# Performance work log

Measured on AMD Instinct MI355X. Metric: run time of the kernel, lower is better.

The kernel has to match this reference:

```python
import jax, jax.numpy as jnp
import numpy as np

Nn, Nt, Np, Ne = 100000, 30000, 400000, 1000000
IN_NODE, IN_NET, IN_PIN, IN_EDGE = 16, 8, 8, 4
H, HP, HE, L, T = 64, 16, 8, 3, 4
LOG2 = 0.6931471805599453  # ShiftedSoftplus shift


def _lrelu(x):
    return jax.nn.leaky_relu(x, 0.01)


def _ssp(x):  # DGL ShiftedSoftplus: softplus(x) - log(2)
    return jax.nn.softplus(x) - LOG2


def _forward(in_node_feat, in_net_feat, in_pin_feat, in_edge_feat,
             pins_src, pins_dst, near_src, near_dst,
             node_lin_W, node_lin_b, net_lin_W, net_lin_b,
             pin_lin_W, pin_lin_b, edge_lin_W, edge_lin_b,
             geom_W, geom_b, pins_W, pins_b,
             cf_node_W, cf_node_b, cf_e1_W, cf_e1_b, cf_e2_W, cf_e2_b,
             cf_out_W, cf_out_b, sage_pool_W, sage_pool_b,
             sage_self_W, sage_neigh_W, sage_bias,
             out1_W, out1_b, out2_W, out2_b, out3_W, out3_b,
             outn1_W, outn1_b, outn2_W, outn2_b, outn3_W, outn3_b):
    node_feat = _lrelu(in_node_feat @ node_lin_W + node_lin_b)   # [Nn,H]
    net_feat = _lrelu(in_net_feat @ net_lin_W + net_lin_b)       # [Nt,H]
    pin_feat = _lrelu(in_pin_feat @ pin_lin_W + pin_lin_b)       # [Np,HP]
    edge_feat = _lrelu(in_edge_feat @ edge_lin_W + edge_lin_b)   # [Ne,HE]

    # static degree norms for GraphConv(norm='both') on 'pins' (node->net)
    ones_p = jnp.ones((Np,), jnp.float32)
    deg_out = jax.ops.segment_sum(ones_p, pins_src, num_segments=Nn)
    deg_in = jax.ops.segment_sum(ones_p, pins_dst, num_segments=Nt)
    src_norm = jnp.clip(deg_out, 1.0, None) ** -0.5
    dst_norm = jnp.clip(deg_in, 1.0, None) ** -0.5

    for i in range(L):
        # --- 'pins' GraphConv (node -> net), norm='both' ---
        msg = (node_feat * src_norm[:, None])[pins_src]                 # [Np,H]
        agg = jax.ops.segment_sum(msg, pins_dst, num_segments=Nt)      # [Nt,H]
        net_out = (agg * dst_norm[:, None]) @ pins_W[i] + pins_b[i]

        # --- 'pinned' CFConv (net -> node), reverse pins, edge feats = pin_feat ---
        hv = net_feat @ cf_node_W[i] + cf_node_b[i]                    # [Nt,H]
        he = _ssp(pin_feat @ cf_e1_W[i] + cf_e1_b[i])
        he = _ssp(he @ cf_e2_W[i] + cf_e2_b[i])                        # [Np,H]
        m = hv[pins_dst] * he                                          # src of 'pinned' = pins_dst
        h_cf = jax.ops.segment_sum(m, pins_src, num_segments=Nn)       # dst of 'pinned' = pins_src
        node_cf = _ssp(h_cf @ cf_out_W[i] + cf_out_b[i])

        # --- 'near' SAGEConv(pool) with sigmoid edge weights ---
        ew = jax.nn.sigmoid(edge_feat @ geom_W[i] + geom_b[i])         # [Ne,1]
        hp = jax.nn.relu(node_feat @ sage_pool_W[i] + sage_pool_b[i])  # [Nn,H]
        m2 = hp[near_src] * ew                                         # [Ne,H], nonnegative
        h_neigh = jax.ops.segment_max(m2, near_dst, num_segments=Nn)
        h_neigh = jnp.maximum(h_neigh, 0.0)  # zero-degree nodes -> 0 (msgs are >= 0)
        node_sage = node_feat @ sage_self_W[i] + h_neigh @ sage_neigh_W[i] + sage_bias[i]

        # hetero max-aggregation over edge types hitting dst 'node'
        node_feat = _lrelu(jnp.maximum(node_cf, node_sage))
        net_feat = _lrelu(net_out)

    h = _lrelu(jnp.concatenate([in_node_feat, node_feat], axis=-1) @ out1_W + out1_b)
    h = _lrelu(h @ out2_W + out2_b)
    node_pred = jax.nn.sigmoid(h @ out3_W + out3_b)
    g = _lrelu(jnp.concatenate([in_net_feat, net_feat], axis=-1) @ outn1_W + outn1_b)
    g = _lrelu(g @ outn2_W + outn2_b)
    net_pred = jax.nn.sigmoid(g @ outn3_W + outn3_b)
    return node_pred, net_pred


def setup_inputs() -> dict:
    key = jax.random.key(0)
    ks = iter(jax.random.split(key, 80))

    def nrm(shape, scale=0.05):
        return jax.random.normal(next(ks), shape, jnp.float32) * scale

    inp = {}
    inp['in_node_feat'] = nrm((Nn, IN_NODE), 1.0)
    inp['in_net_feat'] = nrm((Nt, IN_NET), 1.0)
    inp['in_pin_feat'] = nrm((Np, IN_PIN), 1.0)
    inp['in_edge_feat'] = nrm((Ne, IN_EDGE), 1.0)
    inp['pins_src'] = jax.random.randint(next(ks), (Np,), 0, Nn)
    inp['pins_dst'] = jax.random.randint(next(ks), (Np,), 0, Nt)
    inp['near_src'] = jax.random.randint(next(ks), (Ne,), 0, Nn)
    inp['near_dst'] = jax.random.randint(next(ks), (Ne,), 0, Nn)
    inp['node_lin_W'] = nrm((IN_NODE, H)); inp['node_lin_b'] = nrm((H,))
    inp['net_lin_W'] = nrm((IN_NET, H)); inp['net_lin_b'] = nrm((H,))
    inp['pin_lin_W'] = nrm((IN_PIN, HP)); inp['pin_lin_b'] = nrm((HP,))
    inp['edge_lin_W'] = nrm((IN_EDGE, HE)); inp['edge_lin_b'] = nrm((HE,))
    inp['geom_W'] = nrm((L, HE, 1)); inp['geom_b'] = nrm((L, 1))
    inp['pins_W'] = nrm((L, H, H)); inp['pins_b'] = nrm((L, H))
    inp['cf_node_W'] = nrm((L, H, H)); inp['cf_node_b'] = nrm((L, H))
    inp['cf_e1_W'] = nrm((L, HP, H)); inp['cf_e1_b'] = nrm((L, H))
    inp['cf_e2_W'] = nrm((L, H, H)); inp['cf_e2_b'] = nrm((L, H))
    inp['cf_out_W'] = nrm((L, H, H)); inp['cf_out_b'] = nrm((L, H))
    inp['sage_pool_W'] = nrm((L, H, H)); inp['sage_pool_b'] = nrm((L, H))
    inp['sage_self_W'] = nrm((L, H, H))
    inp['sage_neigh_W'] = nrm((L, H, H))
    inp['sage_bias'] = nrm((L, H))
    inp['out1_W'] = nrm((IN_NODE + H, H)); inp['out1_b'] = nrm((H,))
    inp['out2_W'] = nrm((H, H)); inp['out2_b'] = nrm((H,))
    inp['out3_W'] = nrm((H, T)); inp['out3_b'] = nrm((T,))
    inp['outn1_W'] = nrm((IN_NET + H, H)); inp['outn1_b'] = nrm((H,))
    inp['outn2_W'] = nrm((H, H)); inp['outn2_b'] = nrm((H,))
    inp['outn3_W'] = nrm((H, 1)); inp['outn3_b'] = nrm((1,))
    return inp


def reference(in_node_feat, in_net_feat, in_pin_feat, in_edge_feat,
              pins_src, pins_dst, near_src, near_dst,
              node_lin_W, node_lin_b, net_lin_W, net_lin_b,
              pin_lin_W, pin_lin_b, edge_lin_W, edge_lin_b,
              geom_W, geom_b, pins_W, pins_b,
              cf_node_W, cf_node_b, cf_e1_W, cf_e1_b, cf_e2_W, cf_e2_b,
              cf_out_W, cf_out_b, sage_pool_W, sage_pool_b,
              sage_self_W, sage_neigh_W, sage_bias,
              out1_W, out1_b, out2_W, out2_b, out3_W, out3_b,
              outn1_W, outn1_b, outn2_W, outn2_b, outn3_W, outn3_b):
    return _forward(in_node_feat, in_net_feat, in_pin_feat, in_edge_feat,
                    pins_src, pins_dst, near_src, near_dst,
                    node_lin_W, node_lin_b, net_lin_W, net_lin_b,
                    pin_lin_W, pin_lin_b, edge_lin_W, edge_lin_b,
                    geom_W, geom_b, pins_W, pins_b,
                    cf_node_W, cf_node_b, cf_e1_W, cf_e1_b, cf_e2_W, cf_e2_b,
                    cf_out_W, cf_out_b, sage_pool_W, sage_pool_b,
                    sage_self_W, sage_neigh_W, sage_bias,
                    out1_W, out1_b, out2_W, out2_b, out3_W, out3_b,
                    outn1_W, outn1_b, outn2_W, outn2_b, outn3_W, outn3_b)
```

## Files before the change

### kernel.cpp

```cpp
#include <hip/hip_runtime.h>
#include <hip/hip_bf16.h>

#define DEV __device__ __forceinline__

DEV float lrelu_(float x){ return x > 0.f ? x : 0.01f * x; }
DEV float ssp_(float x){ return fmaxf(x, 0.f) + __logf(1.f + __expf(-fabsf(x))) - 0.69314718055994530942f; }
DEV float sigm_(float x){ return 1.f / (1.f + __expf(-x)); }

DEV unsigned short f2bf(float x){
    unsigned int u = __float_as_uint(x);
    unsigned int r = (u + 0x7FFFu + ((u >> 16) & 1u)) >> 16;
    return (unsigned short)r;
}
DEV float bf2f(unsigned short s){ return __uint_as_float((unsigned int)s << 16); }
DEV ushort4 pack4(float4 v){
    ushort4 u; u.x = f2bf(v.x); u.y = f2bf(v.y); u.z = f2bf(v.z); u.w = f2bf(v.w); return u;
}

DEV void fma44(float (&acc)[4][4], const float4 (&xa)[4], const float4 (&wa)[4])
{
    #pragma unroll
    for (int kk = 0; kk < 4; kk++) {
        #pragma unroll
        for (int i = 0; i < 4; i++) {
            float x = ((const float*)&xa[i])[kk];
            #pragma unroll
            for (int j = 0; j < 4; j++)
                acc[i][j] += x * ((const float*)&wa[kk])[j];
        }
    }
}

typedef short s8v __attribute__((ext_vector_type(8)));
typedef float f4v __attribute__((ext_vector_type(4)));

template<int K, int ACT, bool OUTBF>
__global__ __launch_bounds__(256) void gemm64_kernel(const float* __restrict__ X,
                                                     const float* __restrict__ W,
                                                     const float* __restrict__ B,
                                                     void* __restrict__ Yv, int nrows)
{
    constexpr int XS = K + 4;
    constexpr int KQ = K / 4;
    __shared__ float Ws[K * 64];
    __shared__ float bs[64];
    __shared__ float Xs[64 * XS];
    for (int i = threadIdx.x; i < K * 64; i += 256) Ws[i] = W[i];
    if (threadIdx.x < 64) bs[threadIdx.x] = B[threadIdx.x];
    const int tr = threadIdx.x >> 4, tc = threadIdx.x & 15;
    const int r0 = tr * 4, c0 = tc * 4;
    for (int base = blockIdx.x * 64; base < nrows; base += gridDim.x * 64) {
        __syncthreads();
        for (int i = threadIdx.x; i < 64 * KQ; i += 256) {
            int row = i / KQ, kq = (i % KQ) * 4;
            int g = base + row;
            float4 v = make_float4(0.f, 0.f, 0.f, 0.f);
            if (g < nrows) v = *(const float4*)&X[(size_t)g * K + kq];
            *(float4*)&Xs[row * XS + kq] = v;
        }
        __syncthreads();
        float acc[4][4];
        #pragma unroll
        for (int i = 0; i < 4; i++)
            #pragma unroll
            for (int j = 0; j < 4; j++) acc[i][j] = bs[c0 + j];
        #pragma unroll 4
        for (int kq = 0; kq < K; kq += 4) {
            float4 xa[4], wa[4];
            #pragma unroll
            for (int i = 0; i < 4; i++) xa[i] = *(const float4*)&Xs[(r0 + i) * XS + kq];
            #pragma unroll
            for (int j = 0; j < 4; j++) wa[j] = *(const float4*)&Ws[(kq + j) * 64 + c0];
            fma44(acc, xa, wa);
        }
        #pragma unroll
        for (int i = 0; i < 4; i++) {
            int g = base + r0 + i;
            if (g < nrows) {
                float4 o;
                float* op = (float*)&o;
                #pragma unroll
                for (int j = 0; j < 4; j++) {
                    float a = acc[i][j];
                    if (ACT == 1) a = lrelu_(a);
                    else if (ACT == 2) a = fmaxf(a, 0.f);
                    op[j] = a;
                }
                if (OUTBF) *(ushort4*)&((unsigned short*)Yv)[(size_t)g * 64 + c0] = pack4(o);
                else       *(float4*)&((float*)Yv)[(size_t)g * 64 + c0] = o;
            }
        }
    }
}

template<int ACT, bool INBF, bool OUTBF>
__global__ __launch_bounds__(256) void mfma_gemm_kernel(const void* __restrict__ Xv,
                                                        const float* __restrict__ W,
                                                        const float* __restrict__ B,
                                                        void* __restrict__ Yv, int nrows)
{
    __shared__ __align__(16) unsigned short WT[64 * 72];
    __shared__ __align__(16) unsigned short Axs[64 * 72];
    __shared__ float bs[64];
    for (int i = threadIdx.x; i < 4096; i += 256) {
        int k = i >> 6, nn = i & 63;
        WT[nn * 72 + k] = f2bf(W[i]);
    }
    if (threadIdx.x < 64) bs[threadIdx.x] = B[threadIdx.x];
    const int lane = threadIdx.x & 63, wv = threadIdx.x >> 6;
    const int l15 = lane & 15, quad = lane >> 4;
    const int arow = 16 * wv + l15;
    const int koff = quad * 8;
    for (int base = blockIdx.x * 64; base < nrows; base += gridDim.x * 64) {
        __syncthreads();
        {
            int row = threadIdx.x >> 2, kq = (threadIdx.x & 3) * 16;
            int g = base + row;
            if (INBF) {
                const unsigned short* Xb = (const unsigned short*)Xv;
                uint4 v0 = make_uint4(0,0,0,0), v1 = v0;
                if (g < nrows) {
                    v0 = *(const uint4*)&Xb[(size_t)g * 64 + kq];
                    v1 = *(const uint4*)&Xb[(size_t)g * 64 + kq + 8];
                }
                *(uint4*)&Axs[row * 72 + kq] = v0;
                *(uint4*)&Axs[row * 72 + kq + 8] = v1;
            } else {
                const float* Xf = (const float*)Xv;
                #pragma unroll
                for (int m = 0; m < 4; m++) {
                    float4 v = make_float4(0,0,0,0);
                    if (g < nrows) v = *(const float4*)&Xf[(size_t)g * 64 + kq + m * 4];
                    *(ushort4*)&Axs[row * 72 + kq + m * 4] = pack4(v);
                }
            }
        }
        __syncthreads();
        f4v acc[4];
        #pragma unroll
        for (int t = 0; t < 4; t++) acc[t] = (f4v){0.f,0.f,0.f,0.f};
        s8v a0 = *(const s8v*)&Axs[arow * 72 + koff];
        s8v a1 = *(const s8v*)&Axs[arow * 72 + 32 + koff];
        #pragma unroll
        for (int t = 0; t < 4; t++) {
            int nn = t * 16 + l15;
            s8v b0 = *(const s8v*)&WT[nn * 72 + koff];
            s8v b1 = *(const s8v*)&WT[nn * 72 + 32 + koff];
            acc[t] = __builtin_amdgcn_mfma_f32_16x16x32_bf16(a0, b0, acc[t], 0, 0, 0);
            acc[t] = __builtin_amdgcn_mfma_f32_16x16x32_bf16(a1, b1, acc[t], 0, 0, 0);
        }
        const int mrow = 16 * wv + quad * 4;
        #pragma unroll
        for (int t = 0; t < 4; t++) {
            int col = t * 16 + l15;
            float b = bs[col];
            #pragma unroll
            for (int r = 0; r < 4; r++) {
                int g = base + mrow + r;
                if (g < nrows) {
                    float a = acc[t][r] + b;
                    if (ACT == 1) a = lrelu_(a);
                    else if (ACT == 2) a = fmaxf(a, 0.f);
                    if (OUTBF) ((unsigned short*)Yv)[(size_t)g * 64 + col] = f2bf(a);
                    else       ((float*)Yv)[(size_t)g * 64 + col] = a;
                }
            }
        }
    }
}

__global__ __launch_bounds__(256) void mfma_combine_kernel(const float* __restrict__ h_cf,
                                                           const unsigned short* __restrict__ nfb,
                                                           const unsigned short* __restrict__ ngb,
                                                           const float* __restrict__ Wc, const float* __restrict__ cB,
                                                           const float* __restrict__ sW, const float* __restrict__ nW,
                                                           const float* __restrict__ sB,
                                                           unsigned short* __restrict__ outb, int n)
{
    __shared__ __align__(16) unsigned short WcT[64 * 72], WsT[64 * 72], WnT[64 * 72];
    __shared__ __align__(16) unsigned short Ac[32 * 72], As[32 * 72], An[32 * 72];
    __shared__ float bc[64], bsg[64];
    for (int i = threadIdx.x; i < 4096; i += 256) {
        int k = i >> 6, nn = i & 63;
        WcT[nn * 72 + k] = f2bf(Wc[i]);
        WsT[nn * 72 + k] = f2bf(sW[i]);
        WnT[nn * 72 + k] = f2bf(nW[i]);
    }
    if (threadIdx.x < 64) { bc[threadIdx.x] = cB[threadIdx.x]; bsg[threadIdx.x] = sB[threadIdx.x]; }
    const int lane = threadIdx.x & 63, wv = threadIdx.x >> 6;
    const int l15 = lane & 15, quad = lane >> 4;
    const int arow = (wv & 1) * 16 + l15;
    const int ct0 = (wv >> 1) * 2;
    const int koff = quad * 8;
    for (int base = blockIdx.x * 32; base < n; base += gridDim.x * 32) {
        __syncthreads();
        {
            int row = threadIdx.x >> 3, kq = (threadIdx.x & 7) * 8;
            int g = base + row;
            float4 c0v = make_float4(0,0,0,0), c1 = c0v;
            uint4 vf = make_uint4(0,0,0,0), vg = vf;
            if (g < n) {
                const float* pc = &h_cf[(size_t)g * 64 + kq];
                c0v = *(const float4*)pc; c1 = *(const float4*)(pc + 4);
                vf = *(const uint4*)&nfb[(size_t)g * 64 + kq];
                vg = *(const uint4*)&ngb[(size_t)g * 64 + kq];
            }
            *(ushort4*)&Ac[row * 72 + kq] = pack4(c0v);
            *(ushort4*)&Ac[row * 72 + kq + 4] = pack4(c1);
            *(uint4*)&As[row * 72 + kq] = vf;
            *(uint4*)&An[row * 72 + kq] = vg;
        }
        __syncthreads();
        f4v accC[2], accS[2];
        #pragma unroll
        for (int t = 0; t < 2; t++) { accC[t] = (f4v){0.f,0.f,0.f,0.f}; accS[t] = (f4v){0.f,0.f,0.f,0.f}; }
        s8v ac0 = *(const s8v*)&Ac[arow * 72 + koff];
        s8v ac1 = *(const s8v*)&Ac[arow * 72 + 32 + koff];
        s8v as0 = *(const s8v*)&As[arow * 72 + koff];
        s8v as1 = *(const s8v*)&As[arow * 72 + 32 + koff];
        s8v an0 = *(const s8v*)&An[arow * 72 + koff];
        s8v an1 = *(const s8v*)&An[arow * 72 + 32 + koff];
        #pragma unroll
        for (int t = 0; t < 2; t++) {
            int nn = (ct0 + t) * 16 + l15;
            s8v wc0 = *(const s8v*)&WcT[nn * 72 + koff];
            s8v wc1 = *(const s8v*)&WcT[nn * 72 + 32 + koff];
            accC[t] = __builtin_amdgcn_mfma_f32_16x16x32_bf16(ac0, wc0, accC[t], 0, 0, 0);
            accC[t] = __builtin_amdgcn_mfma_f32_16x16x32_bf16(ac1, wc1, accC[t], 0, 0, 0);
            s8v ws0 = *(const s8v*)&WsT[nn * 72 + koff];
            s8v ws1 = *(const s8v*)&WsT[nn * 72 + 32 + koff];
            accS[t] = __builtin_amdgcn_mfma_f32_16x16x32_bf16(as0, ws0, accS[t], 0, 0, 0);
            accS[t] = __builtin_amdgcn_mfma_f32_16x16x32_bf16(as1, ws1, accS[t], 0, 0, 0);
            s8v wn0 = *(const s8v*)&WnT[nn * 72 + koff];
            s8v wn1 = *(const s8v*)&WnT[nn * 72 + 32 + koff];
            accS[t] = __builtin_amdgcn_mfma_f32_16x16x32_bf16(an0, wn0, accS[t], 0, 0, 0);
            accS[t] = __builtin_amdgcn_mfma_f32_16x16x32_bf16(an1, wn1, accS[t], 0, 0, 0);
        }
        const int mrow = (wv & 1) * 16 + quad * 4;
        #pragma unroll
        for (int t = 0; t < 2; t++) {
            int col = (ct0 + t) * 16 + l15;
            float bcv = bc[col], bsv = bsg[col];
            #pragma unroll
            for (int r = 0; r < 4; r++) {
                int g = base + mrow + r;
                if (g < n)
                    outb[(size_t)g * 64 + col] = f2bf(lrelu_(fmaxf(ssp_(accC[t][r] + bcv), accS[t][r] + bsv)));
            }
        }
    }
}

template<int K, int C, int ACT>
__global__ __launch_bounds__(256) void lin_kernel(const float* __restrict__ X,
                                                  const float* __restrict__ W,
                                                  const float* __restrict__ B,
                                                  float* __restrict__ Y, int nrows)
{
    constexpr int ROWS = 256 / C;
    __shared__ float Ws[K * C];
    __shared__ float bs[C];
    __shared__ float Xs[ROWS * K];
    for (int i = threadIdx.x; i < K * C; i += 256) Ws[i] = W[i];
    if (threadIdx.x < C) bs[threadIdx.x] = B[threadIdx.x];
    __syncthreads();
    const int r = threadIdx.x / C, c = threadIdx.x % C;
    for (int base = blockIdx.x * ROWS; base < nrows; base += gridDim.x * ROWS) {
        __syncthreads();
        for (int i = threadIdx.x; i < ROWS * K; i += 256) {
            int rr = base + i / K;
            Xs[i] = (rr < nrows) ? X[(size_t)rr * K + i % K] : 0.f;
        }
        __syncthreads();
        int row = base + r;
        if (row < nrows) {
            float acc = bs[c];
            #pragma unroll
            for (int k = 0; k < K; k++) acc += Xs[r * K + k] * Ws[k * C + c];
            if (ACT == 1) acc = lrelu_(acc);
            else if (ACT == 2) acc = fmaxf(acc, 0.f);
            Y[(size_t)row * C + c] = acc;
        }
    }
}

__global__ __launch_bounds__(256) void deg_kernel(const int* __restrict__ src, const int* __restrict__ dst,
                                                  int* __restrict__ degs, int* __restrict__ degd, int np)
{
    int p = blockIdx.x * 256 + threadIdx.x;
    if (p < np) { atomicAdd(&degs[src[p]], 1); atomicAdd(&degd[dst[p]], 1); }
}

__global__ __launch_bounds__(256) void norm_kernel(int* __restrict__ arr, int n)
{
    int i = blockIdx.x * 256 + threadIdx.x;
    if (i < n) {
        int v = arr[i]; if (v < 1) v = 1;
        arr[i] = __float_as_int(rsqrtf((float)v));
    }
}

__global__ __launch_bounds__(256) void csr_count_kernel(const int* __restrict__ key, int* __restrict__ cnt, int ne)
{
    int e = blockIdx.x * 256 + threadIdx.x;
    if (e < ne) atomicAdd(&cnt[key[e]], 1);
}

__global__ __launch_bounds__(256) void scan_block_sum_kernel(const int* __restrict__ cnt, int* __restrict__ bsum, int n)
{
    __shared__ int sh[256];
    int i = blockIdx.x * 256 + threadIdx.x;
    sh[threadIdx.x] = (i < n) ? cnt[i] : 0;
    __syncthreads();
    for (int s = 128; s > 0; s >>= 1) {
        if (threadIdx.x < s) sh[threadIdx.x] += sh[threadIdx.x + s];
        __syncthreads();
    }
    if (threadIdx.x == 0) bsum[blockIdx.x] = sh[0];
}

__global__ __launch_bounds__(512) void scan_bsum_kernel(int* __restrict__ bsum, int nb, int* __restrict__ total_out)
{
    __shared__ int sh[512];
    int i = threadIdx.x;
    int v = (i < nb) ? bsum[i] : 0;
    sh[i] = v;
    __syncthreads();
    for (int s = 1; s < 512; s <<= 1) {
        int add = (i >= s) ? sh[i - s] : 0;
        __syncthreads();
        sh[i] += add;
        __syncthreads();
    }
    if (i < nb) bsum[i] = sh[i] - v;
    if (i == nb - 1) *total_out = sh[i];
}

__global__ __launch_bounds__(256) void scan_final_kernel(const int* __restrict__ cnt, const int* __restrict__ bsum,
                                                         int* __restrict__ row_start, int* __restrict__ nxt, int n)
{
    __shared__ int sh[256];
    int i = blockIdx.x * 256 + threadIdx.x;
    int v = (i < n) ? cnt[i] : 0;
    sh[threadIdx.x] = v;
    __syncthreads();
    for (int s = 1; s < 256; s <<= 1) {
        int add = (threadIdx.x >= s) ? sh[threadIdx.x - s] : 0;
        __syncthreads();
        sh[threadIdx.x] += add;
        __syncthreads();
    }
    if (i < n) {
        int excl = sh[threadIdx.x] - v + bsum[blockIdx.x];
        row_start[i] = excl;
        nxt[i] = excl;
    }
}

__global__ __launch_bounds__(256) void csr_fill_kernel(const int* __restrict__ key, int* __restrict__ nxt,
                                                       int* __restrict__ eidx, int ne)
{
    int e = blockIdx.x * 256 + threadIdx.x;
    if (e < ne) {
        int slot = atomicAdd(&nxt[key[e]], 1);
        eidx[slot] = e;
    }
}

__global__ __launch_bounds__(256) void edge_ew_kernel(const float* __restrict__ in_edge,
                                                      const float* __restrict__ elW, const float* __restrict__ elb,
                                                      const float* __restrict__ gW, const float* __restrict__ gb,
                                                      float* __restrict__ ew3, int ne)
{
    __shared__ float W[32], B[8], G[24], Gb[3];
    if (threadIdx.x < 32) W[threadIdx.x] = elW[threadIdx.x];
    if (threadIdx.x < 8)  B[threadIdx.x] = elb[threadIdx.x];
    if (threadIdx.x < 24) G[threadIdx.x] = gW[threadIdx.x];
    if (threadIdx.x < 3)  Gb[threadIdx.x] = gb[threadIdx.x];
    __syncthreads();
    for (int e = blockIdx.x * 256 + threadIdx.x; e < ne; e += gridDim.x * 256) {
        float4 x = *(const float4*)&in_edge[(size_t)e * 4];
        float ef[8];
        #pragma unroll
        for (int j = 0; j < 8; j++)
            ef[j] = lrelu_(B[j] + x.x * W[j] + x.y * W[8 + j] + x.z * W[16 + j] + x.w * W[24 + j]);
        #pragma unroll
        for (int i = 0; i < 3; i++) {
            float a = Gb[i];
            #pragma unroll
            for (int j = 0; j < 8; j++) a += ef[j] * G[i * 8 + j];
            ew3[(size_t)i * ne + e] = sigm_(a);
        }
    }
}

__global__ __launch_bounds__(256) void pins_gather_kernel(const unsigned short* __restrict__ nfb,
                                                          const float* __restrict__ snorm,
                                                          const float* __restrict__ dnorm,
                                                          const int* __restrict__ psrc,
                                                          const int* __restrict__ prow,
                                                          const int* __restrict__ peidx,
                                                          unsigned short* __restrict__ aggb, int nt)
{
    __shared__ int sS[4][64];
    __shared__ float sN[4][64];
    const int lane = threadIdx.x & 63, wv = threadIdx.x >> 6;
    for (int d = blockIdx.x * 4 + wv; d < nt; d += gridDim.x * 4) {
        int rs = prow[d], re = prow[d + 1];
        float acc = 0.f;
        for (int cbase = rs; cbase < re; cbase += 64) {
            int cnt = re - cbase; if (cnt > 64) cnt = 64;
            if (lane < cnt) {
                int p = peidx[cbase + lane];
                int s = psrc[p];
                sS[wv][lane] = s;
                sN[wv][lane] = snorm[s];
            }
            int k = 0;
            for (; k + 3 < cnt; k += 4) {
                int s0 = sS[wv][k], s1 = sS[wv][k+1], s2 = sS[wv][k+2], s3 = sS[wv][k+3];
                float n0 = sN[wv][k], n1 = sN[wv][k+1], n2 = sN[wv][k+2], n3 = sN[wv][k+3];
                float v0 = bf2f(nfb[(size_t)s0 * 64 + lane]) * n0;
                float v1 = bf2f(nfb[(size_t)s1 * 64 + lane]) * n1;
                float v2 = bf2f(nfb[(size_t)s2 * 64 + lane]) * n2;
                float v3 = bf2f(nfb[(size_t)s3 * 64 + lane]) * n3;
                acc += (v0 + v1) + (v2 + v3);
            }
            for (; k < cnt; k++)
                acc += bf2f(nfb[(size_t)sS[wv][k] * 64 + lane]) * sN[wv][k];
        }
        aggb[(size_t)d * 64 + lane] = f2bf(acc * dnorm[d]);
    }
}

__global__ __launch_bounds__(256) void cf_pin5_kernel(const float* __restrict__ pinf,
                                                      const unsigned short* __restrict__ hvb,
                                                      const int* __restrict__ psrc, const int* __restrict__ pdst,
                                                      const float* __restrict__ W1, const float* __restrict__ B1,
                                                      const float* __restrict__ W2, const float* __restrict__ B2,
                                                      float* __restrict__ h_cf, int np)
{
    __shared__ float Ws1[16 * 64], bs1[64], bs2[64];
    __shared__ __align__(16) unsigned short W2T[64 * 72];
    __shared__ __align__(16) unsigned short T1s[64 * 72];
    __shared__ float PF[64 * 20];
    __shared__ int srcS[64], dstS[64];
    for (int i = threadIdx.x; i < 16 * 64; i += 256) Ws1[i] = W1[i];
    for (int i = threadIdx.x; i < 64 * 64; i += 256) {
        int k = i >> 6, n = i & 63;
        W2T[n * 72 + k] = f2bf(W2[i]);
    }
    if (threadIdx.x < 64) { bs1[threadIdx.x] = B1[threadIdx.x]; bs2[threadIdx.x] = B2[threadIdx.x]; }
    const int tr = threadIdx.x >> 4, tc = threadIdx.x & 15;
    const int r0 = tr * 4, c0 = tc * 4;
    const int lane = threadIdx.x & 63, wv = threadIdx.x >> 6;
    const int l15 = lane & 15, quad = lane >> 4;
    const int arow = 16 * wv + l15;
    const int koff = quad * 8;
    for (int base = blockIdx.x * 64; base < np; base += gridDim.x * 64) {
        __syncthreads();
        {
            int row = threadIdx.x >> 2, kq = (threadIdx.x & 3) * 4;
            int p = base + row;
            float4 v = make_float4(0.f, 0.f, 0.f, 0.f);
            if (p < np) v = *(const float4*)&pinf[(size_t)p * 16 + kq];
            *(float4*)&PF[row * 20 + kq] = v;
            if (threadIdx.x < 64) {
                int pp = base + threadIdx.x;
                srcS[threadIdx.x] = (pp < np) ? psrc[pp] : 0;
                dstS[threadIdx.x] = (pp < np) ? pdst[pp] : 0;
            }
        }
        __syncthreads();
        {
            float acc[4][4];
            #pragma unroll
            for (int i = 0; i < 4; i++)
                #pragma unroll
                for (int j = 0; j < 4; j++) acc[i][j] = bs1[c0 + j];
            #pragma unroll
            for (int kq = 0; kq < 16; kq += 4) {
                float4 xa[4], wa[4];
                #pragma unroll
                for (int i = 0; i < 4; i++) xa[i] = *(const float4*)&PF[(r0 + i) * 20 + kq];
                #pragma unroll
                for (int j = 0; j < 4; j++) wa[j] = *(const float4*)&Ws1[(kq + j) * 64 + c0];
                fma44(acc, xa, wa);
            }
            #pragma unroll
            for (int i = 0; i < 4; i++) {
                ushort4 o;
                o.x = f2bf(ssp_(acc[i][0]));
                o.y = f2bf(ssp_(acc[i][1]));
                o.z = f2bf(ssp_(acc[i][2]));
                o.w = f2bf(ssp_(acc[i][3]));
                *(ushort4*)&T1s[(r0 + i) * 72 + c0] = o;
            }
        }
        __syncthreads();
        {
            f4v acc4[4];
            #pragma unroll
            for (int t = 0; t < 4; t++) acc4[t] = (f4v){0.f, 0.f, 0.f, 0.f};
            s8v a0 = *(const s8v*)&T1s[arow * 72 + koff];
            s8v a1 = *(const s8v*)&T1s[arow * 72 + 32 + koff];
            #pragma unroll
            for (int t = 0; t < 4; t++) {
                int n = t * 16 + l15;
                s8v b0 = *(const s8v*)&W2T[n * 72 + koff];
                s8v b1 = *(const s8v*)&W2T[n * 72 + 32 + koff];
                acc4[t] = __builtin_amdgcn_mfma_f32_16x16x32_bf16(a0, b0, acc4[t], 0, 0, 0);
                acc4[t] = __builtin_amdgcn_mfma_f32_16x16x32_bf16(a1, b1, acc4[t], 0, 0, 0);
            }
            __syncthreads();
            const int mrow = 16 * wv + quad * 4;
            #pragma unroll
            for (int t = 0; t < 4; t++) {
                int col = t * 16 + l15;
                float b = bs2[col];
                #pragma unroll
                for (int r = 0; r < 4; r++)
                    T1s[(mrow + r) * 72 + col] = f2bf(ssp_(acc4[t][r] + b));
            }
        }
        __syncthreads();
        #pragma unroll 4
        for (int i = 0; i < 16; i++) {
            int pl = wv * 16 + i;
            int p = base + pl;
            if (p < np) {
                float m = bf2f(hvb[(size_t)dstS[pl] * 64 + lane]) * bf2f(T1s[pl * 72 + lane]);
                unsafeAtomicAdd(&h_cf[(size_t)srcS[pl] * 64 + lane], m);
            }
        }
    }
}

__global__ __launch_bounds__(256) void sage_gather_kernel(const unsigned short* __restrict__ hpb,
                                                          const float* __restrict__ ew,
                                                          const int* __restrict__ esrc,
                                                          const int* __restrict__ row_start,
                                                          const int* __restrict__ eidx,
                                                          unsigned short* __restrict__ ngb, int nn)
{
    __shared__ int sS[4][64];
    __shared__ float sWt[4][64];
    const int lane = threadIdx.x & 63, wv = threadIdx.x >> 6;
    for (int d = blockIdx.x * 4 + wv; d < nn; d += gridDim.x * 4) {
        int rs = row_start[d], re = row_start[d + 1];
        float acc = 0.f;
        for (int cbase = rs; cbase < re; cbase += 64) {
            int cnt = re - cbase; if (cnt > 64) cnt = 64;
            if (lane < cnt) {
                int e = eidx[cbase + lane];
                sS[wv][lane] = esrc[e];
                sWt[wv][lane] = ew[e];
            }
            int k = 0;
            for (; k + 3 < cnt; k += 4) {
                int s0 = sS[wv][k], s1 = sS[wv][k+1], s2 = sS[wv][k+2], s3 = sS[wv][k+3];
                float w0 = sWt[wv][k], w1 = sWt[wv][k+1], w2 = sWt[wv][k+2], w3 = sWt[wv][k+3];
                float v0 = bf2f(hpb[(size_t)s0 * 64 + lane]) * w0;
                float v1 = bf2f(hpb[(size_t)s1 * 64 + lane]) * w1;
                float v2 = bf2f(hpb[(size_t)s2 * 64 + lane]) * w2;
                float v3 = bf2f(hpb[(size_t)s3 * 64 + lane]) * w3;
                acc = fmaxf(acc, fmaxf(fmaxf(v0, v1), fmaxf(v2, v3)));
            }
            for (; k < cnt; k++)
                acc = fmaxf(acc, bf2f(hpb[(size_t)sS[wv][k] * 64 + lane]) * sWt[wv][k]);
        }
        ngb[(size_t)d * 64 + lane] = f2bf(acc);
    }
}

__global__ __launch_bounds__(256) void node_head3_kernel(const float* __restrict__ in_node,
                                                         const unsigned short* __restrict__ nfb,
                                                         const float* __restrict__ W1, const float* __restrict__ B1,
                                                         const float* __restrict__ W2, const float* __restrict__ B2,
                                                         const float* __restrict__ W3, const float* __restrict__ B3,
                                                         float* __restrict__ out, int n)
{
    __shared__ float Ws1[80 * 64], Ws2[64 * 64], Ws3[64 * 4];
    __shared__ float bs1[64], bs2[64], bs3[4];
    __shared__ float Xs[32 * 84];
    __shared__ float H1[32 * 68];
    for (int i = threadIdx.x; i < 80 * 64; i += 256) Ws1[i] = W1[i];
    for (int i = threadIdx.x; i < 64 * 64; i += 256) Ws2[i] = W2[i];
    for (int i = threadIdx.x; i < 64 * 4; i += 256) Ws3[i] = W3[i];
    if (threadIdx.x < 64) { bs1[threadIdx.x] = B1[threadIdx.x]; bs2[threadIdx.x] = B2[threadIdx.x]; }
    if (threadIdx.x < 4) bs3[threadIdx.x] = B3[threadIdx.x];
    const int tr = threadIdx.x >> 4, tc = threadIdx.x & 15;
    const int r0 = tr * 2, c0 = tc * 4;
    for (int base = blockIdx.x * 32; base < n; base += gridDim.x * 32) {
        __syncthreads();
        for (int i = threadIdx.x; i < 32 * 4; i += 256) {
            int row = i >> 2, kq = (i & 3) * 4;
            int g = base + row;
            float4 v = make_float4(0,0,0,0);
            if (g < n) v = *(const float4*)&in_node[(size_t)g * 16 + kq];
            *(float4*)&Xs[row * 84 + kq] = v;
        }
        for (int i = threadIdx.x; i < 32 * 16; i += 256) {
            int row = i >> 4, kq = (i & 15) * 4;
            int g = base + row;
            float4 v = make_float4(0,0,0,0);
            if (g < n) {
                ushort4 u = *(const ushort4*)&nfb[(size_t)g * 64 + kq];
                v.x = bf2f(u.x); v.y = bf2f(u.y); v.z = bf2f(u.z); v.w = bf2f(u.w);
            }
            *(float4*)&Xs[row * 84 + 16 + kq] = v;
        }
        __syncthreads();
        {
            float acc[2][4];
            #pragma unroll
            for (int i = 0; i < 2; i++)
                #pragma unroll
                for (int j = 0; j < 4; j++) acc[i][j] = bs1[c0 + j];
            #pragma unroll 4
            for (int kq = 0; kq < 80; kq += 4) {
                float4 xa[2], wa[4];
                #pragma unroll
                for (int i = 0; i < 2; i++) xa[i] = *(const float4*)&Xs[(r0 + i) * 84 + kq];
                #pragma unroll
                for (int j = 0; j < 4; j++) wa[j] = *(const float4*)&Ws1[(kq + j) * 64 + c0];
                #pragma unroll
                for (int kk = 0; kk < 4; kk++)
                    #pragma unroll
                    for (int i = 0; i < 2; i++) {
                        float x = ((const float*)&xa[i])[kk];
                        #pragma unroll
                        for (int j = 0; j < 4; j++) acc[i][j] += x * ((const float*)&wa[kk])[j];
                    }
            }
            #pragma unroll
            for (int i = 0; i < 2; i++) {
                float4 o; float* op = (float*)&o;
                #pragma unroll
                for (int j = 0; j < 4; j++) op[j] = lrelu_(acc[i][j]);
                *(float4*)&H1[(r0 + i) * 68 + c0] = o;
            }
        }
        __syncthreads();
        float* H2 = Xs;
        {
            float acc[2][4];
            #pragma unroll
            for (int i = 0; i < 2; i++)
                #pragma unroll
                for (int j = 0; j < 4; j++) acc[i][j] = bs2[c0 + j];
            #pragma unroll 4
            for (int kq = 0; kq < 64; kq += 4) {
                float4 xa[2], wa[4];
                #pragma unroll
                for (int i = 0; i < 2; i++) xa[i] = *(const float4*)&H1[(r0 + i) * 68 + kq];
                #pragma unroll
                for (int j = 0; j < 4; j++) wa[j] = *(const float4*)&Ws2[(kq + j) * 64 + c0];
                #pragma unroll
                for (int kk = 0; kk < 4; kk++)
                    #pragma unroll
                    for (int i = 0; i < 2; i++) {
                        float x = ((const float*)&xa[i])[kk];
                        #pragma unroll
                        for (int j = 0; j < 4; j++) acc[i][j] += x * ((const float*)&wa[kk])[j];
                    }
            }
            __syncthreads();
            #pragma unroll
            for (int i = 0; i < 2; i++) {
                float4 o; float* op = (float*)&o;
                #pragma unroll
                for (int j = 0; j < 4; j++) op[j] = lrelu_(acc[i][j]);
                *(float4*)&H2[(r0 + i) * 68 + c0] = o;
            }
        }
        __syncthreads();
        if (threadIdx.x < 128) {
            int row = threadIdx.x >> 2, c = threadIdx.x & 3;
            float acc = bs3[c];
            #pragma unroll 4
            for (int kq = 0; kq < 64; kq += 4) {
                float4 h = *(const float4*)&H2[row * 68 + kq];
                #pragma unroll
                for (int j = 0; j < 4; j++) acc += ((const float*)&h)[j] * Ws3[(kq + j) * 4 + c];
            }
            int g = base + row;
            if (g < n) out[(size_t)g * 4 + c] = sigm_(acc);
        }
    }
}

__global__ __launch_bounds__(256) void net_head3_kernel(const float* __restrict__ in_net, const float* __restrict__ tf,
                                                        const float* __restrict__ W1, const float* __restrict__ B1,
                                                        const float* __restrict__ W2, const float* __restrict__ B2,
                                                        const float* __restrict__ W3, const float* __restrict__ B3,
                                                        float* __restrict__ out, int n)
{
    __shared__ float Ws1[72 * 64], Ws2[64 * 64], Ws3[64];
    __shared__ float bs1[64], bs2[64], bs3[1];
    __shared__ float Xs[32 * 76];
    __shared__ float H1[32 * 68];
    for (int i = threadIdx.x; i < 72 * 64; i += 256) Ws1[i] = W1[i];
    for (int i = threadIdx.x; i < 64 * 64; i += 256) Ws2[i] = W2[i];
    if (threadIdx.x < 64) { Ws3[threadIdx.x] = W3[threadIdx.x]; bs1[threadIdx.x] = B1[threadIdx.x]; bs2[threadIdx.x] = B2[threadIdx.x]; }
    if (threadIdx.x == 0) bs3[0] = B3[0];
    const int tr = threadIdx.x >> 4, tc = threadIdx.x & 15;
    const int r0 = tr * 2, c0 = tc * 4;
    for (int base = blockIdx.x * 32; base < n; base += gridDim.x * 32) {
        __syncthreads();
        for (int i = threadIdx.x; i < 32 * 2; i += 256) {
            int row = i >> 1, kq = (i & 1) * 4;
            int g = base + row;
            float4 v = make_float4(0,0,0,0);
            if (g < n) v = *(const float4*)&in_net[(size_t)g * 8 + kq];
            *(float4*)&Xs[row * 76 + kq] = v;
        }
        for (int i = threadIdx.x; i < 32 * 16; i += 256) {
            int row = i >> 4, kq = (i & 15) * 4;
            int g = base + row;
            float4 v = make_float4(0,0,0,0);
            if (g < n) v = *(const float4*)&tf[(size_t)g * 64 + kq];
            *(float4*)&Xs[row * 76 + 8 + kq] = v;
        }
        __syncthreads();
        {
            float acc[2][4];
            #pragma unroll
            for (int i = 0; i < 2; i++)
                #pragma unroll
                for (int j = 0; j < 4; j++) acc[i][j] = bs1[c0 + j];
            #pragma unroll 4
            for (int kq = 0; kq < 72; kq += 4) {
                float4 xa[2], wa[4];
                #pragma unroll
                for (int i = 0; i < 2; i++) xa[i] = *(const float4*)&Xs[(r0 + i) * 76 + kq];
                #pragma unroll
                for (int j = 0; j < 4; j++) wa[j] = *(const float4*)&Ws1[(kq + j) * 64 + c0];
                #pragma unroll
                for (int kk = 0; kk < 4; kk++)
                    #pragma unroll
                    for (int i = 0; i < 2; i++) {
                        float x = ((const float*)&xa[i])[kk];
                        #pragma unroll
                        for (int j = 0; j < 4; j++) acc[i][j] += x * ((const float*)&wa[kk])[j];
                    }
            }
            #pragma unroll
            for (int i = 0; i < 2; i++) {
                float4 o; float* op = (float*)&o;
                #pragma unroll
                for (int j = 0; j < 4; j++) op[j] = lrelu_(acc[i][j]);
                *(float4*)&H1[(r0 + i) * 68 + c0] = o;
            }
        }
        __syncthreads();
        float* H2 = Xs;
        {
            float acc[2][4];
            #pragma unroll
            for (int i = 0; i < 2; i++)
                #pragma unroll
                for (int j = 0; j < 4; j++) acc[i][j] = bs2[c0 + j];
            #pragma unroll 4
            for (int kq = 0; kq < 64; kq += 4) {
                float4 xa[2], wa[4];
                #pragma unroll
                for (int i = 0; i < 2; i++) xa[i] = *(const float4*)&H1[(r0 + i) * 68 + kq];
                #pragma unroll
                for (int j = 0; j < 4; j++) wa[j] = *(const float4*)&Ws2[(kq + j) * 64 + c0];
                #pragma unroll
                for (int kk = 0; kk < 4; kk++)
                    #pragma unroll
                    for (int i = 0; i < 2; i++) {
                        float x = ((const float*)&xa[i])[kk];
                        #pragma unroll
                        for (int j = 0; j < 4; j++) acc[i][j] += x * ((const float*)&wa[kk])[j];
                    }
            }
            __syncthreads();
            #pragma unroll
            for (int i = 0; i < 2; i++) {
                float4 o; float* op = (float*)&o;
                #pragma unroll
                for (int j = 0; j < 4; j++) op[j] = lrelu_(acc[i][j]);
                *(float4*)&H2[(r0 + i) * 68 + c0] = o;
            }
        }
        __syncthreads();
        if (threadIdx.x < 32) {
            int row = threadIdx.x;
            float acc = bs3[0];
            #pragma unroll 4
            for (int kq = 0; kq < 64; kq += 4) {
                float4 h = *(const float4*)&H2[row * 68 + kq];
                float4 w = *(const float4*)&Ws3[kq];
                acc += h.x * w.x + h.y * w.y + h.z * w.z + h.w * w.w;
            }
            int g = base + row;
            if (g < n) out[g] = sigm_(acc);
        }
    }
}

extern "C" void kernel_launch(void* const* d_in, const int* in_sizes, int n_in,
                              void* d_out, int out_size, void* d_ws, size_t ws_size,
                              hipStream_t stream)
{
    (void)in_sizes; (void)n_in; (void)out_size; (void)ws_size;
    constexpr int Nn = 100000, Nt = 30000, Np = 400000, Ne = 1000000;
    constexpr int H = 64, L = 3, T = 4;

    auto fpt = [&](int i){ return (const float*)d_in[i]; };
    auto ipt = [&](int i){ return (const int*)d_in[i]; };

    const float* in_node = fpt(0);
    const float* in_net  = fpt(1);
    const float* in_pin  = fpt(2);
    const float* in_edge = fpt(3);
    const int* psrc = ipt(4);
    const int* pdst = ipt(5);
    const int* esrc = ipt(6);
    const int* edst = ipt(7);

    float* ws = (float*)d_ws;
    size_t o = 0;
    auto alloc = [&](size_t nel){ float* p = ws + o; o += nel; return p; };
    unsigned short* node_a = (unsigned short*)alloc((size_t)Nn * 32);
    unsigned short* node_b = (unsigned short*)alloc((size_t)Nn * 32);
    unsigned short* aggb   = (unsigned short*)alloc((size_t)Nt * 32);
    unsigned short* hvb    = (unsigned short*)alloc((size_t)Nt * 32);
    unsigned short* hpb    = (unsigned short*)alloc((size_t)Nn * 32);
    unsigned short* ngb    = (unsigned short*)alloc((size_t)Nn * 32);
    float* net_a  = alloc((size_t)Nt * H);
    float* net_b  = alloc((size_t)Nt * H);
    float* pinf   = alloc((size_t)Np * 16);
    float* h_cf   = alloc((size_t)Nn * H);
    float* ew3    = alloc((size_t)3 * Ne);
    float* snorm  = alloc((size_t)Nn);
    float* dnorm  = alloc((size_t)Nt);
    int* cnt       = (int*)alloc((size_t)Nn);
    int* row_start = (int*)alloc((size_t)Nn + 1);
    int* nxt       = (int*)alloc((size_t)Nn);
    int* eidx      = (int*)alloc((size_t)Ne);
    int* bsum      = (int*)alloc((size_t)512);
    int* pcnt      = (int*)alloc((size_t)Nt);
    int* prow      = (int*)alloc((size_t)Nt + 1);
    int* pnxt      = (int*)alloc((size_t)Nt);
    int* peidx     = (int*)alloc((size_t)Np);
    int* pbsum     = (int*)alloc((size_t)256);

    constexpr int NB  = (Nn + 255) / 256;
    constexpr int NB2 = (Nt + 255) / 256;

    hipMemsetAsync(snorm, 0, (size_t)Nn * 4, stream);
    hipMemsetAsync(dnorm, 0, (size_t)Nt * 4, stream);
    deg_kernel<<<(Np + 255) / 256, 256, 0, stream>>>(psrc, pdst, (int*)snorm, (int*)dnorm, Np);
    norm_kernel<<<(Nn + 255) / 256, 256, 0, stream>>>((int*)snorm, Nn);
    norm_kernel<<<(Nt + 255) / 256, 256, 0, stream>>>((int*)dnorm, Nt);

    hipMemsetAsync(cnt, 0, (size_t)Nn * 4, stream);
    csr_count_kernel<<<(Ne + 255) / 256, 256, 0, stream>>>(edst, cnt, Ne);
    scan_block_sum_kernel<<<NB, 256, 0, stream>>>(cnt, bsum, Nn);
    scan_bsum_kernel<<<1, 512, 0, stream>>>(bsum, NB, row_start + Nn);
    scan_final_kernel<<<NB, 256, 0, stream>>>(cnt, bsum, row_start, nxt, Nn);
    csr_fill_kernel<<<(Ne + 255) / 256, 256, 0, stream>>>(edst, nxt, eidx, Ne);

    hipMemsetAsync(pcnt, 0, (size_t)Nt * 4, stream);
    csr_count_kernel<<<(Np + 255) / 256, 256, 0, stream>>>(pdst, pcnt, Np);
    scan_block_sum_kernel<<<NB2, 256, 0, stream>>>(pcnt, pbsum, Nt);
    scan_bsum_kernel<<<1, 512, 0, stream>>>(pbsum, NB2, prow + Nt);
    scan_final_kernel<<<NB2, 256, 0, stream>>>(pcnt, pbsum, prow, pnxt, Nt);
    csr_fill_kernel<<<(Np + 255) / 256, 256, 0, stream>>>(pdst, pnxt, peidx, Np);

    gemm64_kernel<16, 1, true><<<1024, 256, 0, stream>>>(in_node, fpt(8),  fpt(9),  node_a, Nn);
    gemm64_kernel< 8, 1, false><<<469, 256, 0, stream>>>(in_net,  fpt(10), fpt(11), net_a,  Nt);
    lin_kernel<8, 16, 1><<<1024, 256, 0, stream>>>(in_pin, fpt(12), fpt(13), pinf, Np);
    edge_ew_kernel<<<2048, 256, 0, stream>>>(in_edge, fpt(14), fpt(15), fpt(16), fpt(17), ew3, Ne);

    unsigned short* ncur = node_a; unsigned short* nnew = node_b;
    float* tcur = net_a;  float* tnew = net_b;

    for (int i = 0; i < L; i++) {
        pins_gather_kernel<<<(Nt + 3) / 4, 256, 0, stream>>>(ncur, snorm, dnorm, psrc, prow, peidx, aggb, Nt);
        mfma_gemm_kernel<1, true, false><<<469, 256, 0, stream>>>(aggb, fpt(18) + (size_t)i * 4096, fpt(19) + (size_t)i * 64, tnew, Nt);

        mfma_gemm_kernel<0, false, true><<<469, 256, 0, stream>>>(tcur, fpt(20) + (size_t)i * 4096, fpt(21) + (size_t)i * 64, hvb, Nt);
        hipMemsetAsync(h_cf, 0, (size_t)Nn * H * 4, stream);
        cf_pin5_kernel<<<1024, 256, 0, stream>>>(pinf, hvb, psrc, pdst,
                                                 fpt(22) + (size_t)i * 1024, fpt(23) + (size_t)i * 64,
                                                 fpt(24) + (size_t)i * 4096, fpt(25) + (size_t)i * 64,
                                                 h_cf, Np);

        mfma_gemm_kernel<2, true, true><<<1024, 256, 0, stream>>>(ncur, fpt(28) + (size_t)i * 4096, fpt(29) + (size_t)i * 64, hpb, Nn);
        sage_gather_kernel<<<(Nn + 3) / 4, 256, 0, stream>>>(hpb, ew3 + (size_t)i * Ne, esrc, row_start, eidx, ngb, Nn);

        mfma_combine_kernel<<<1024, 256, 0, stream>>>(h_cf, ncur, ngb,
                                                      fpt(26) + (size_t)i * 4096, fpt(27) + (size_t)i * 64,
                                                      fpt(30) + (size_t)i * 4096, fpt(31) + (size_t)i * 4096,
                                                      fpt(32) + (size_t)i * 64,
                                                      nnew, Nn);

        unsigned short* t = ncur; ncur = nnew; nnew = t;
        float* tf = tcur; tcur = tnew; tnew = tf;
    }

    float* out = (float*)d_out;
    node_head3_kernel<<<640, 256, 0, stream>>>(in_node, ncur, fpt(33), fpt(34), fpt(35), fpt(36), fpt(37), fpt(38), out, Nn);
    net_head3_kernel<<<480, 256, 0, stream>>>(in_net, tcur, fpt(39), fpt(40), fpt(41), fpt(42), fpt(43), fpt(44), out + (size_t)Nn * T, Nt);
}
```

Baseline: 1.140 ms.

## Replace CFConv atomic scatter with CSR gather by source node

The pin-edge MLP kernel now writes per-pin edge weights to a bf16 buffer instead of atomically scattering fp32 messages into node rows. A new CSR keyed on pin source is built once, and a per-node gather kernel sums hv[dst]*he into a bf16 output. The first edge linear layer also moves from FP32 FMA to MFMA. This removes the atomics, the per-layer memset and the fp32 intermediate. In exchange it adds an HEb write and read round trip (400k x 64 bf16 per layer), extra CSR setup, and bf16 rounding of the aggregate.

```diff
diff --git a/kernel.cpp b/kernel.cpp
--- a/kernel.cpp
+++ b/kernel.cpp
@@ -169,7 +169,7 @@
     }
 }
 
-__global__ __launch_bounds__(256) void mfma_combine_kernel(const float* __restrict__ h_cf,
+__global__ __launch_bounds__(256) void mfma_combine_kernel(const unsigned short* __restrict__ cfb,
                                                            const unsigned short* __restrict__ nfb,
                                                            const unsigned short* __restrict__ ngb,
                                                            const float* __restrict__ Wc, const float* __restrict__ cB,
@@ -197,16 +197,13 @@
         {
             int row = threadIdx.x >> 3, kq = (threadIdx.x & 7) * 8;
             int g = base + row;
-            float4 c0v = make_float4(0,0,0,0), c1 = c0v;
-            uint4 vf = make_uint4(0,0,0,0), vg = vf;
+            uint4 vc = make_uint4(0,0,0,0), vf = vc, vg = vc;
             if (g < n) {
-                const float* pc = &h_cf[(size_t)g * 64 + kq];
-                c0v = *(const float4*)pc; c1 = *(const float4*)(pc + 4);
+                vc = *(const uint4*)&cfb[(size_t)g * 64 + kq];
                 vf = *(const uint4*)&nfb[(size_t)g * 64 + kq];
                 vg = *(const uint4*)&ngb[(size_t)g * 64 + kq];
             }
-            *(ushort4*)&Ac[row * 72 + kq] = pack4(c0v);
-            *(ushort4*)&Ac[row * 72 + kq + 4] = pack4(c1);
+            *(uint4*)&Ac[row * 72 + kq] = vc;
             *(uint4*)&As[row * 72 + kq] = vf;
             *(uint4*)&An[row * 72 + kq] = vg;
         }
@@ -433,30 +430,30 @@
     }
 }
 
-__global__ __launch_bounds__(256) void cf_pin5_kernel(const float* __restrict__ pinf,
-                                                      const unsigned short* __restrict__ hvb,
-                                                      const int* __restrict__ psrc, const int* __restrict__ pdst,
+__global__ __launch_bounds__(256) void cf_pin6_kernel(const float* __restrict__ pinf,
                                                       const float* __restrict__ W1, const float* __restrict__ B1,
                                                       const float* __restrict__ W2, const float* __restrict__ B2,
-                                                      float* __restrict__ h_cf, int np)
-{
-    __shared__ float Ws1[16 * 64], bs1[64], bs2[64];
+                                                      unsigned short* __restrict__ HEb, int np)
+{
+    __shared__ __align__(16) unsigned short W1T[64 * 40];
     __shared__ __align__(16) unsigned short W2T[64 * 72];
+    __shared__ __align__(16) unsigned short PFb[64 * 40];
     __shared__ __align__(16) unsigned short T1s[64 * 72];
-    __shared__ float PF[64 * 20];
-    __shared__ int srcS[64], dstS[64];
-    for (int i = threadIdx.x; i < 16 * 64; i += 256) Ws1[i] = W1[i];
-    for (int i = threadIdx.x; i < 64 * 64; i += 256) {
+    __shared__ float bs1[64], bs2[64];
+    for (int i = threadIdx.x; i < 64 * 32; i += 256) {
+        int n = i & 63, k = i >> 6;
+        W1T[n * 40 + k] = (k < 16) ? f2bf(W1[k * 64 + n]) : (unsigned short)0;
+    }
+    for (int i = threadIdx.x; i < 4096; i += 256) {
         int k = i >> 6, n = i & 63;
         W2T[n * 72 + k] = f2bf(W2[i]);
     }
     if (threadIdx.x < 64) { bs1[threadIdx.x] = B1[threadIdx.x]; bs2[threadIdx.x] = B2[threadIdx.x]; }
-    const int tr = threadIdx.x >> 4, tc = threadIdx.x & 15;
-    const int r0 = tr * 4, c0 = tc * 4;
     const int lane = threadIdx.x & 63, wv = threadIdx.x >> 6;
     const int l15 = lane & 15, quad = lane >> 4;
     const int arow = 16 * wv + l15;
     const int koff = quad * 8;
+    const int mrow = 16 * wv + quad * 4;
     for (int base = blockIdx.x * 64; base < np; base += gridDim.x * 64) {
         __syncthreads();
         {
@@ -464,37 +461,29 @@
             int p = base + row;
             float4 v = make_float4(0.f, 0.f, 0.f, 0.f);
             if (p < np) v = *(const float4*)&pinf[(size_t)p * 16 + kq];
-            *(float4*)&PF[row * 20 + kq] = v;
-            if (threadIdx.x < 64) {
-                int pp = base + threadIdx.x;
-                srcS[threadIdx.x] = (pp < np) ? psrc[pp] : 0;
-                dstS[threadIdx.x] = (pp < np) ? pdst[pp] : 0;
-            }
+            *(ushort4*)&PFb[row * 40 + kq] = pack4(v);
+            if ((threadIdx.x & 3) < 2)
+                *(uint4*)&PFb[row * 40 + 16 + (threadIdx.x & 3) * 8] = make_uint4(0,0,0,0);
         }
         __syncthreads();
         {
-            float acc[4][4];
-            #pragma unroll
-            for (int i = 0; i < 4; i++)
-                #pragma unroll
-                for (int j = 0; j < 4; j++) acc[i][j] = bs1[c0 + j];
-            #pragma unroll
-            for (int kq = 0; kq < 16; kq += 4) {
-                float4 xa[4], wa[4];
-                #pragma unroll
-                for (int i = 0; i < 4; i++) xa[i] = *(const float4*)&PF[(r0 + i) * 20 + kq];
-                #pragma unroll
-                for (int j = 0; j < 4; j++) wa[j] = *(const float4*)&Ws1[(kq + j) * 64 + c0];
-                fma44(acc, xa, wa);
-            }
-            #pragma unroll
-            for (int i = 0; i < 4; i++) {
-                ushort4 o;
-                o.x = f2bf(ssp_(acc[i][0]));
-                o.y = f2bf(ssp_(acc[i][1]));
-                o.z = f2bf(ssp_(acc[i][2]));
-                o.w = f2bf(ssp_(acc[i][3]));
-                *(ushort4*)&T1s[(r0 + i) * 72 + c0] = o;
+            f4v acc1[4];
+            #pragma unroll
+            for (int t = 0; t < 4; t++) acc1[t] = (f4v){0.f,0.f,0.f,0.f};
+            s8v a = *(const s8v*)&PFb[arow * 40 + koff];
+            #pragma unroll
+            for (int t = 0; t < 4; t++) {
+                int n = t * 16 + l15;
+                s8v b = *(const s8v*)&W1T[n * 40 + koff];
+                acc1[t] = __builtin_amdgcn_mfma_f32_16x16x32_bf16(a, b, acc1[t], 0, 0, 0);
+            }
+            #pragma unroll
+            for (int t = 0; t < 4; t++) {
+                int col = t * 16 + l15;
+                float b = bs1[col];
+                #pragma unroll
+                for (int r = 0; r < 4; r++)
+                    T1s[(mrow + r) * 72 + col] = f2bf(ssp_(acc1[t][r] + b));
             }
         }
         __syncthreads();
@@ -513,7 +502,6 @@
                 acc4[t] = __builtin_amdgcn_mfma_f32_16x16x32_bf16(a1, b1, acc4[t], 0, 0, 0);
             }
             __syncthreads();
-            const int mrow = 16 * wv + quad * 4;
             #pragma unroll
             for (int t = 0; t < 4; t++) {
                 int col = t * 16 + l15;
@@ -524,15 +512,52 @@
             }
         }
         __syncthreads();
-        #pragma unroll 4
-        for (int i = 0; i < 16; i++) {
-            int pl = wv * 16 + i;
-            int p = base + pl;
+        {
+            int row = threadIdx.x >> 2, kq = (threadIdx.x & 3) * 16;
+            int p = base + row;
             if (p < np) {
-                float m = bf2f(hvb[(size_t)dstS[pl] * 64 + lane]) * bf2f(T1s[pl * 72 + lane]);
-                unsafeAtomicAdd(&h_cf[(size_t)srcS[pl] * 64 + lane], m);
-            }
-        }
+                *(uint4*)&HEb[(size_t)p * 64 + kq]     = *(const uint4*)&T1s[row * 72 + kq];
+                *(uint4*)&HEb[(size_t)p * 64 + kq + 8] = *(const uint4*)&T1s[row * 72 + kq + 8];
+            }
+        }
+    }
+}
+
+__global__ __launch_bounds__(256) void cf_gather_kernel(const unsigned short* __restrict__ HEb,
+                                                        const unsigned short* __restrict__ hvb,
+                                                        const int* __restrict__ pdst,
+                                                        const int* __restrict__ srow,
+                                                        const int* __restrict__ seidx,
+                                                        unsigned short* __restrict__ cfb, int nn)
+{
+    __shared__ int sP[4][64], sD[4][64];
+    const int lane = threadIdx.x & 63, wv = threadIdx.x >> 6;
+    for (int d = blockIdx.x * 4 + wv; d < nn; d += gridDim.x * 4) {
+        int rs = srow[d], re = srow[d + 1];
+        float acc = 0.f;
+        for (int cbase = rs; cbase < re; cbase += 64) {
+            int cnt = re - cbase; if (cnt > 64) cnt = 64;
+            if (lane < cnt) {
+                int p = seidx[cbase + lane];
+                sP[wv][lane] = p;
+                sD[wv][lane] = pdst[p];
+            }
+            int k = 0;
+            for (; k + 1 < cnt; k += 2) {
+                int p0 = sP[wv][k], p1 = sP[wv][k+1];
+                int d0 = sD[wv][k], d1 = sD[wv][k+1];
+                float he0 = bf2f(HEb[(size_t)p0 * 64 + lane]);
+                float hv0 = bf2f(hvb[(size_t)d0 * 64 + lane]);
+                float he1 = bf2f(HEb[(size_t)p1 * 64 + lane]);
+                float hv1 = bf2f(hvb[(size_t)d1 * 64 + lane]);
+                acc += he0 * hv0 + he1 * hv1;
+            }
+            if (k < cnt) {
+                int p0 = sP[wv][k], d0 = sD[wv][k];
+                acc += bf2f(HEb[(size_t)p0 * 64 + lane]) * bf2f(hvb[(size_t)d0 * 64 + lane]);
+            }
+        }
+        cfb[(size_t)d * 64 + lane] = f2bf(acc);
     }
 }
 
@@ -831,10 +856,11 @@
     unsigned short* hvb    = (unsigned short*)alloc((size_t)Nt * 32);
     unsigned short* hpb    = (unsigned short*)alloc((size_t)Nn * 32);
     unsigned short* ngb    = (unsigned short*)alloc((size_t)Nn * 32);
+    unsigned short* HEb    = (unsigned short*)alloc((size_t)Np * 32);
+    unsigned short* cfb    = (unsigned short*)alloc((size_t)Nn * 32);
     float* net_a  = alloc((size_t)Nt * H);
     float* net_b  = alloc((size_t)Nt * H);
     float* pinf   = alloc((size_t)Np * 16);
-    float* h_cf   = alloc((size_t)Nn * H);
     float* ew3    = alloc((size_t)3 * Ne);
     float* snorm  = alloc((size_t)Nn);
     float* dnorm  = alloc((size_t)Nt);
@@ -848,6 +874,8 @@
     int* pnxt      = (int*)alloc((size_t)Nt);
     int* peidx     = (int*)alloc((size_t)Np);
     int* pbsum     = (int*)alloc((size_t)256);
+    int* srow      = (int*)alloc((size_t)Nn + 1);
+    int* seidx     = (int*)alloc((size_t)Np);
 
     constexpr int NB  = (Nn + 255) / 256;
     constexpr int NB2 = (Nt + 255) / 256;
@@ -872,6 +900,13 @@
     scan_final_kernel<<<NB2, 256, 0, stream>>>(pcnt, pbsum, prow, pnxt, Nt);
     csr_fill_kernel<<<(Np + 255) / 256, 256, 0, stream>>>(pdst, pnxt, peidx, Np);
 
+    hipMemsetAsync(cnt, 0, (size_t)Nn * 4, stream);
+    csr_count_kernel<<<(Np + 255) / 256, 256, 0, stream>>>(psrc, cnt, Np);
+    scan_block_sum_kernel<<<NB, 256, 0, stream>>>(cnt, bsum, Nn);
+    scan_bsum_kernel<<<1, 512, 0, stream>>>(bsum, NB, srow + Nn);
+    scan_final_kernel<<<NB, 256, 0, stream>>>(cnt, bsum, srow, nxt, Nn);
+    csr_fill_kernel<<<(Np + 255) / 256, 256, 0, stream>>>(psrc, nxt, seidx, Np);
+
     gemm64_kernel<16, 1, true><<<1024, 256, 0, stream>>>(in_node, fpt(8),  fpt(9),  node_a, Nn);
     gemm64_kernel< 8, 1, false><<<469, 256, 0, stream>>>(in_net,  fpt(10), fpt(11), net_a,  Nt);
     lin_kernel<8, 16, 1><<<1024, 256, 0, stream>>>(in_pin, fpt(12), fpt(13), pinf, Np);
@@ -885,16 +920,16 @@
         mfma_gemm_kernel<1, true, false><<<469, 256, 0, stream>>>(aggb, fpt(18) + (size_t)i * 4096, fpt(19) + (size_t)i * 64, tnew, Nt);
 
         mfma_gemm_kernel<0, false, true><<<469, 256, 0, stream>>>(tcur, fpt(20) + (size_t)i * 4096, fpt(21) + (size_t)i * 64, hvb, Nt);
-        hipMemsetAsync(h_cf, 0, (size_t)Nn * H * 4, stream);
-        cf_pin5_kernel<<<1024, 256, 0, stream>>>(pinf, hvb, psrc, pdst,
+        cf_pin6_kernel<<<1024, 256, 0, stream>>>(pinf,
                                                  fpt(22) + (size_t)i * 1024, fpt(23) + (size_t)i * 64,
                                                  fpt(24) + (size_t)i * 4096, fpt(25) + (size_t)i * 64,
-                                                 h_cf, Np);
+                                                 HEb, Np);
+        cf_gather_kernel<<<(Nn + 3) / 4, 256, 0, stream>>>(HEb, hvb, pdst, srow, seidx, cfb, Nn);
 
         mfma_gemm_kernel<2, true, true><<<1024, 256, 0, stream>>>(ncur, fpt(28) + (size_t)i * 4096, fpt(29) + (size_t)i * 64, hpb, Nn);
         sage_gather_kernel<<<(Nn + 3) / 4, 256, 0, stream>>>(hpb, ew3 + (size_t)i * Ne, esrc, row_start, eidx, ngb, Nn);
 
-        mfma_combine_kernel<<<1024, 256, 0, stream>>>(h_cf, ncur, ngb,
+        mfma_combine_kernel<<<1024, 256, 0, stream>>>(cfb, ncur, ngb,
                                                       fpt(26) + (size_t)i * 4096, fpt(27) + (size_t)i * 64,
                                                       fpt(30) + (size_t)i * 4096, fpt(31) + (size_t)i * 4096,
                                                       fpt(32) + (size_t)i * 64,
```

Result: faster. 1.098 ms (-3.7%).
